# Kernel tuning notes

Measured on AMD Instinct MI355X. Metric: run time of the kernel, lower is better.

## Reference

```python
import jax, jax.numpy as jnp
import numpy as np

N = 50000   # num_nodes
E = 1600000 # edges (avg degree 32)
D = 256     # in_feats
H = 256     # n_hidden


def setup_inputs() -> dict:
    key = jax.random.key(0)
    ks = jax.random.split(key, 9)
    s = 1.0 / np.sqrt(D)
    return {
        "input_nodes": jnp.arange(N, dtype=jnp.int32),
        "edge_src": jax.random.randint(ks[0], (E,), 0, N, dtype=jnp.int32),
        "edge_dst": jax.random.randint(ks[1], (E,), 0, N, dtype=jnp.int32),
        "emb": jax.random.normal(ks[2], (N, D), jnp.float32) * 0.02,
        "W_self0": jax.random.normal(ks[3], (D, H), jnp.float32) * s,
        "W_neigh0": jax.random.normal(ks[4], (D, H), jnp.float32) * s,
        "b0": jnp.zeros((H,), jnp.float32),
        "W_self1": jax.random.normal(ks[5], (H, H), jnp.float32) * s,
        "W_neigh1": jax.random.normal(ks[6], (H, H), jnp.float32) * s,
        "b1": jnp.zeros((H,), jnp.float32),
    }


def _sage_mean(h, src, dst, W_self, W_neigh, b, n):
    # gather neighbor features, mean-reduce by destination, then linear.
    msgs = h[src]                                                  # [E, d]
    ssum = jax.ops.segment_sum(msgs, dst, num_segments=n)          # [n, d]
    deg = jax.ops.segment_sum(jnp.ones(src.shape, h.dtype), dst, num_segments=n)
    h_neigh = ssum / jnp.maximum(deg, 1.0)[:, None]
    return h @ W_self + h_neigh @ W_neigh + b


def reference(input_nodes, edge_src, edge_dst, emb,
              W_self0, W_neigh0, b0, W_self1, W_neigh1, b1):
    h = emb[input_nodes]                                            # [N, D]
    h = _sage_mean(h, edge_src, edge_dst, W_self0, W_neigh0, b0, N)
    h = jax.nn.relu(h)  # dropout is identity at inference
    h = _sage_mean(h, edge_src, edge_dst, W_self1, W_neigh1, b1, N)
    h = h / jnp.linalg.norm(h)  # global Frobenius norm, as in torch.norm(h)
    return h
```

## Files before the change

kernel.cpp:

```cpp
#include <hip/hip_runtime.h>
#include <math.h>

#define NN 50000
#define NE 1600000
#define DF 256
#define NBUCK 391

typedef unsigned short ushortT;
typedef __attribute__((ext_vector_type(8))) short short8;
typedef __attribute__((ext_vector_type(4))) float floatx4;

__device__ __forceinline__ unsigned bf16rne(float f) {
    unsigned u = __float_as_uint(f);
    return (u + 0x7fffu + ((u >> 16) & 1u)) >> 16;
}

#define ASYNC16(gptr, ldsptr) \
    __builtin_amdgcn_global_load_lds((const __attribute__((address_space(1))) unsigned*)(gptr), \
                                     (__attribute__((address_space(3))) unsigned*)(ldsptr), 16, 0, 0)


__global__ void k_zero(int* __restrict__ bcnt) {
    int i = blockIdx.x * 256 + threadIdx.x;
    if (i < NBUCK) bcnt[i] = 0;
}

__global__ __launch_bounds__(256)
void k_bhist(const int* __restrict__ dst, int* __restrict__ bcnt) {
    __shared__ int h[NBUCK];
    for (int i = threadIdx.x; i < NBUCK; i += 256) h[i] = 0;
    __syncthreads();
    int base = blockIdx.x * 4096;
#pragma unroll
    for (int i = 0; i < 16; ++i) {
        int e = base + i * 256 + threadIdx.x;
        if (e < NE) atomicAdd(&h[dst[e] >> 7], 1);
    }
    __syncthreads();
    for (int i = threadIdx.x; i < NBUCK; i += 256)
        if (h[i]) atomicAdd(&bcnt[i], h[i]);
}

__global__ void k_bscan(const int* __restrict__ bcnt, int* __restrict__ bbase,
                        int* __restrict__ cursor, int* __restrict__ row_ptr,
                        float* __restrict__ nrm) {
    __shared__ int s[512];
    int t = threadIdx.x;
    int v = (t < NBUCK) ? bcnt[t] : 0;
    s[t] = v; __syncthreads();
    for (int off = 1; off < 512; off <<= 1) {
        int x = (t >= off) ? s[t - off] : 0;
        __syncthreads();
        s[t] += x;
        __syncthreads();
    }
    if (t < NBUCK) { bbase[t] = s[t] - v; cursor[t] = s[t] - v; }
    if (t == 0) { bbase[NBUCK] = NE; row_ptr[NN] = NE; *nrm = 0.0f; }
}

__global__ __launch_bounds__(256)
void k_bin(const int* __restrict__ src, const int* __restrict__ dst,
           int* __restrict__ cursor, unsigned* __restrict__ rec) {
    __shared__ int h[NBUCK];
    __shared__ int gb[NBUCK];
    for (int i = threadIdx.x; i < NBUCK; i += 256) h[i] = 0;
    __syncthreads();
    const int base = blockIdx.x * 2048;
    int bk[8], rk[8];
    unsigned pk[8];
#pragma unroll
    for (int i = 0; i < 8; ++i) {
        int e = base + i * 256 + threadIdx.x;
        if (e < NE) {
            int d = dst[e];
            bk[i] = d >> 7;
            pk[i] = (unsigned)src[e] | ((unsigned)(d & 127) << 16);
            rk[i] = atomicAdd(&h[bk[i]], 1);
        } else bk[i] = -1;
    }
    __syncthreads();
    for (int i = threadIdx.x; i < NBUCK; i += 256) {
        int c = h[i];
        gb[i] = c ? atomicAdd(&cursor[i], c) : 0;
    }
    __syncthreads();
#pragma unroll
    for (int i = 0; i < 8; ++i)
        if (bk[i] >= 0) rec[gb[bk[i]] + rk[i]] = pk[i];
}

__global__ __launch_bounds__(256)
void k_csr(const unsigned* __restrict__ rec, const int* __restrict__ bbase,
           int* __restrict__ row_ptr, ushortT* __restrict__ csr) {
    __shared__ int cnt[128];
    __shared__ int cur[128];
    __shared__ int s[256];
    const int B = blockIdx.x, t = threadIdx.x;
    if (t < 128) cnt[t] = 0;
    __syncthreads();
    const int beg = bbase[B], end = bbase[B + 1];
    for (int p = beg + t; p < end; p += 256)
        atomicAdd(&cnt[(rec[p] >> 16) & 127], 1);
    __syncthreads();
    int v = (t < 128) ? cnt[t] : 0;
    s[t] = v; __syncthreads();
    for (int off = 1; off < 256; off <<= 1) {
        int x = (t >= off) ? s[t - off] : 0;
        __syncthreads();
        s[t] += x;
        __syncthreads();
    }
    if (t < 128) {
        int ex = s[t] - v;
        cur[t] = ex;
        int node = B * 128 + t;
        if (node < NN) row_ptr[node] = beg + ex;
    }
    __syncthreads();
    for (int p = beg + t; p < end; p += 256) {
        unsigned r = rec[p];
        int loc = atomicAdd(&cur[(r >> 16) & 127], 1);
        csr[beg + loc] = (ushortT)r;
    }
}


__global__ __launch_bounds__(256)
void k_cvt_emb(const float* __restrict__ emb, const int* __restrict__ gather,
               ushortT* __restrict__ out) {
    long long i = ((long long)blockIdx.x * 256 + threadIdx.x) * 8;
    int row = (int)(i >> 8);
    int col = (int)(i & 255);
    long long g = (long long)gather[row] * 256 + col;
    float4 v0 = *(const float4*)(emb + g);
    float4 v1 = *(const float4*)(emb + g + 4);
    uint4 o;
    o.x = bf16rne(v0.x) | (bf16rne(v0.y) << 16);
    o.y = bf16rne(v0.z) | (bf16rne(v0.w) << 16);
    o.z = bf16rne(v1.x) | (bf16rne(v1.y) << 16);
    o.w = bf16rne(v1.z) | (bf16rne(v1.w) << 16);
    *(uint4*)(out + i) = o;
}

__global__ __launch_bounds__(256)
void k_cvt_w(const float* __restrict__ Ws, const float* __restrict__ Wn,
             ushortT* __restrict__ Wt) {
    int idx = blockIdx.x * 256 + threadIdx.x;
    int n = idx >> 9;
    int k = idx & 511;
    float v = (k < 256) ? Ws[k * 256 + n] : Wn[(k - 256) * 256 + n];
    Wt[idx] = (ushortT)bf16rne(v);
}


__global__ __launch_bounds__(256)
void k_agg(const ushortT* __restrict__ feat, const int* __restrict__ row_ptr,
           const ushortT* __restrict__ csr, ushortT* __restrict__ out) {
    int node = blockIdx.x * 4 + (threadIdx.x >> 6);
    int lane = threadIdx.x & 63;
    int half = lane >> 5;
    int l5 = lane & 31;
    if (node >= NN) return;
    int beg = row_ptr[node], end = row_ptr[node + 1];

    float s[8] = {0.f, 0.f, 0.f, 0.f, 0.f, 0.f, 0.f, 0.f};
    int p = beg + half;

#define ACCUM(q) do { \
        s[0] += __uint_as_float(q.x << 16); \
        s[1] += __uint_as_float(q.x & 0xffff0000u); \
        s[2] += __uint_as_float(q.y << 16); \
        s[3] += __uint_as_float(q.y & 0xffff0000u); \
        s[4] += __uint_as_float(q.z << 16); \
        s[5] += __uint_as_float(q.z & 0xffff0000u); \
        s[6] += __uint_as_float(q.w << 16); \
        s[7] += __uint_as_float(q.w & 0xffff0000u); \
    } while (0)

    for (; p + 6 < end; p += 8) {
        long long r0 = (long long)csr[p]     * 256 + l5 * 8;
        long long r1 = (long long)csr[p + 2] * 256 + l5 * 8;
        long long r2 = (long long)csr[p + 4] * 256 + l5 * 8;
        long long r3 = (long long)csr[p + 6] * 256 + l5 * 8;
        uint4 a = *(const uint4*)(feat + r0);
        uint4 b = *(const uint4*)(feat + r1);
        uint4 c = *(const uint4*)(feat + r2);
        uint4 d = *(const uint4*)(feat + r3);
        ACCUM(a); ACCUM(b); ACCUM(c); ACCUM(d);
    }
    for (; p < end; p += 2) {
        long long r0 = (long long)csr[p] * 256 + l5 * 8;
        uint4 a = *(const uint4*)(feat + r0);
        ACCUM(a);
    }
#undef ACCUM

#pragma unroll
    for (int k = 0; k < 8; ++k) s[k] += __shfl_down(s[k], 32);

    if (half == 0) {
        float inv = 1.0f / fmaxf((float)(end - beg), 1.0f);
        uint4 o;
        o.x = bf16rne(s[0] * inv) | (bf16rne(s[1] * inv) << 16);
        o.y = bf16rne(s[2] * inv) | (bf16rne(s[3] * inv) << 16);
        o.z = bf16rne(s[4] * inv) | (bf16rne(s[5] * inv) << 16);
        o.w = bf16rne(s[6] * inv) | (bf16rne(s[7] * inv) << 16);
        *(uint4*)(out + (long long)node * 256 + l5 * 8) = o;
    }
}


template<int RELU, int NORM>
__global__ __launch_bounds__(256, 2)
void k_gemm(const ushortT* __restrict__ Aself, const ushortT* __restrict__ Aneigh,
            const ushortT* __restrict__ Wt, const float* __restrict__ bias,
            ushortT* __restrict__ Cb, float* __restrict__ Cf, float* __restrict__ norm_acc) {
    __shared__ ushortT As[4096];
    __shared__ ushortT Bs[4096];
    __shared__ float red[4];

    const int t = threadIdx.x;
    const int w = t >> 6;
    const int lane = t & 63;
    const int m0 = blockIdx.x * 128;
    const int n0 = blockIdx.y * 128;

    const int r0 = t >> 2;
    const int cu = (t & 3) * 8;

    const long long gA0 = (long long)min(m0 + r0, NN - 1) * 256;
    const long long gA1 = (long long)min(m0 + r0 + 64, NN - 1) * 256;
    const long long gB0 = (long long)(n0 + r0) * 512;
    const long long gB1 = (long long)(n0 + r0 + 64) * 512;

    const unsigned lds0 = w * 512;
    const unsigned lds1 = 2048 + w * 512;

    const int wm = w & 1, wn = w >> 1;
    const int fm = lane & 15;
    const int fk = (lane >> 4) * 8;

    floatx4 acc[4][4];
#pragma unroll
    for (int i = 0; i < 4; ++i)
#pragma unroll
        for (int j = 0; j < 4; ++j) acc[i][j] = (floatx4){0.f, 0.f, 0.f, 0.f};

    for (int kt = 0; kt < 512; kt += 32) {
        const ushortT* Ab; int kc;
        if (kt < 256) { Ab = Aself; kc = kt; } else { Ab = Aneigh; kc = kt - 256; }

        __syncthreads();
        ASYNC16(Ab + gA0 + kc + cu, As + lds0);
        ASYNC16(Ab + gA1 + kc + cu, As + lds1);
        ASYNC16(Wt + gB0 + kt + cu, Bs + lds0);
        ASYNC16(Wt + gB1 + kt + cu, Bs + lds1);
        __syncthreads();

        short8 af[4], bf[4];
#pragma unroll
        for (int i = 0; i < 4; ++i)
            af[i] = *(const short8*)&As[(wm * 64 + i * 16 + fm) * 32 + fk];
#pragma unroll
        for (int j = 0; j < 4; ++j)
            bf[j] = *(const short8*)&Bs[(wn * 64 + j * 16 + fm) * 32 + fk];
#pragma unroll
        for (int i = 0; i < 4; ++i)
#pragma unroll
            for (int j = 0; j < 4; ++j)
                acc[i][j] = __builtin_amdgcn_mfma_f32_16x16x32_bf16(af[i], bf[j], acc[i][j], 0, 0, 0);
    }

    float bj[4];
#pragma unroll
    for (int j = 0; j < 4; ++j) bj[j] = bias[n0 + wn * 64 + j * 16 + fm];

    float sumsq = 0.0f;
#pragma unroll
    for (int i = 0; i < 4; ++i) {
#pragma unroll
        for (int r = 0; r < 4; ++r) {
            const int row = m0 + wm * 64 + i * 16 + (lane >> 4) * 4 + r;
            if (row < NN) {
#pragma unroll
                for (int j = 0; j < 4; ++j) {
                    const int col = n0 + wn * 64 + j * 16 + fm;
                    float v = acc[i][j][r] + bj[j];
                    if (RELU) v = fmaxf(v, 0.0f);
                    if (NORM) {
                        Cf[(long long)row * 256 + col] = v;
                        sumsq += v * v;
                    } else {
                        Cb[(long long)row * 256 + col] = (ushortT)bf16rne(v);
                    }
                }
            }
        }
    }

    if (NORM) {
#pragma unroll
        for (int off = 32; off > 0; off >>= 1) sumsq += __shfl_down(sumsq, off);
        if (lane == 0) red[w] = sumsq;
        __syncthreads();
        if (t == 0) atomicAdd(norm_acc, red[0] + red[1] + red[2] + red[3]);
    }
}

__global__ void k_scale(float* __restrict__ out, const float* __restrict__ nrm) {
    const float s = 1.0f / sqrtf(*nrm);
    long long i = ((long long)blockIdx.x * 256 + threadIdx.x) * 4;
    float4 v = *(float4*)&out[i];
    v.x *= s; v.y *= s; v.z *= s; v.w *= s;
    *(float4*)&out[i] = v;
}


extern "C" void kernel_launch(void* const* d_in, const int* in_sizes, int n_in,
                              void* d_out, int out_size, void* d_ws, size_t ws_size,
                              hipStream_t stream) {
    const int*   input_nodes = (const int*)d_in[0];
    const int*   esrc = (const int*)d_in[1];
    const int*   edst = (const int*)d_in[2];
    const float* emb  = (const float*)d_in[3];
    const float* Ws0  = (const float*)d_in[4];
    const float* Wn0  = (const float*)d_in[5];
    const float* b0   = (const float*)d_in[6];
    const float* Ws1  = (const float*)d_in[7];
    const float* Wn1  = (const float*)d_in[8];
    const float* b1   = (const float*)d_in[9];
    float* out = (float*)d_out;

    char* base = (char*)d_ws;
    ushortT*  embb    = (ushortT*) (base);
    ushortT*  h1b     = (ushortT*) (base + 25600000);
    ushortT*  hnb     = (ushortT*) (base + 51200000);
    unsigned* rec     = (unsigned*)(base + 76800000);
    ushortT*  csr     = (ushortT*) (base + 83200000);
    ushortT*  Wt0     = (ushortT*) (base + 86400000);
    ushortT*  Wt1     = (ushortT*) (base + 86662144);
    int*      row_ptr = (int*)     (base + 86924288);
    int*      bcnt    = (int*)     (base + 87124304);
    int*      bbase   = (int*)     (base + 87125904);
    int*      cursor  = (int*)     (base + 87127504);
    float*    nrm     = (float*)   (base + 87129104);

    k_zero  <<<2,   256, 0, stream>>>(bcnt);
    k_bhist <<<391, 256, 0, stream>>>(edst, bcnt);
    k_bscan <<<1,   512, 0, stream>>>(bcnt, bbase, cursor, row_ptr, nrm);
    k_bin   <<<782, 256, 0, stream>>>(esrc, edst, cursor, rec);
    k_csr   <<<NBUCK, 256, 0, stream>>>(rec, bbase, row_ptr, csr);

    k_cvt_emb<<<NN * DF / 8 / 256, 256, 0, stream>>>(emb, input_nodes, embb);
    k_cvt_w  <<<512, 256, 0, stream>>>(Ws0, Wn0, Wt0);
    k_cvt_w  <<<512, 256, 0, stream>>>(Ws1, Wn1, Wt1);

    dim3 gg((NN + 127) / 128, 2);

    k_agg<<<NN / 4, 256, 0, stream>>>(embb, row_ptr, csr, hnb);
    k_gemm<1, 0><<<gg, 256, 0, stream>>>(embb, hnb, Wt0, b0, h1b, nullptr, nullptr);

    k_agg<<<NN / 4, 256, 0, stream>>>(h1b, row_ptr, csr, hnb);
    k_gemm<0, 1><<<gg, 256, 0, stream>>>(h1b, hnb, Wt1, b1, nullptr, out, nrm);

    k_scale<<<NN * DF / 4 / 256, 256, 0, stream>>>(out, nrm);
}
```

Before: 471.6 us.

## Fuse neighbor mean aggregation into GEMM via LDS-resident aggregated tile

```diff
diff --git a/kernel.cpp b/kernel.cpp
--- a/kernel.cpp
+++ b/kernel.cpp
@@ -153,19 +153,29 @@
 }
 
 
-__global__ __launch_bounds__(256)
-void k_agg(const ushortT* __restrict__ feat, const int* __restrict__ row_ptr,
-           const ushortT* __restrict__ csr, ushortT* __restrict__ out) {
-    int node = blockIdx.x * 4 + (threadIdx.x >> 6);
-    int lane = threadIdx.x & 63;
-    int half = lane >> 5;
-    int l5 = lane & 31;
-    if (node >= NN) return;
-    int beg = row_ptr[node], end = row_ptr[node + 1];
-
-    float s[8] = {0.f, 0.f, 0.f, 0.f, 0.f, 0.f, 0.f, 0.f};
-    int p = beg + half;
-
+template<int RELU, int NORM>
+__global__ __launch_bounds__(256, 2)
+void k_fused(const ushortT* __restrict__ A, const ushortT* __restrict__ Wt,
+             const float* __restrict__ bias, const int* __restrict__ row_ptr,
+             const ushortT* __restrict__ csr,
+             ushortT* __restrict__ Cb, float* __restrict__ Cf,
+             float* __restrict__ norm_acc) {
+    __shared__ ushortT S[40960];
+
+    const int t = threadIdx.x;
+    const int w = t >> 6;
+    const int lane = t & 63;
+    const int half = lane >> 5;
+    const int l5 = lane & 31;
+    const int m0 = blockIdx.x * 128;
+
+    for (int i = 0; i < 32; ++i) {
+        const int nl = w * 32 + i;
+        const int node = m0 + nl;
+        if (node >= NN) break;
+        const int beg = row_ptr[node], end = row_ptr[node + 1];
+        float s[8] = {0.f, 0.f, 0.f, 0.f, 0.f, 0.f, 0.f, 0.f};
+        int p = beg + half;
 #define ACCUM(q) do { \
         s[0] += __uint_as_float(q.x << 16); \
         s[1] += __uint_as_float(q.x & 0xffff0000u); \
@@ -176,122 +186,117 @@
         s[6] += __uint_as_float(q.w << 16); \
         s[7] += __uint_as_float(q.w & 0xffff0000u); \
     } while (0)
-
-    for (; p + 6 < end; p += 8) {
-        long long r0 = (long long)csr[p]     * 256 + l5 * 8;
-        long long r1 = (long long)csr[p + 2] * 256 + l5 * 8;
-        long long r2 = (long long)csr[p + 4] * 256 + l5 * 8;
-        long long r3 = (long long)csr[p + 6] * 256 + l5 * 8;
-        uint4 a = *(const uint4*)(feat + r0);
-        uint4 b = *(const uint4*)(feat + r1);
-        uint4 c = *(const uint4*)(feat + r2);
-        uint4 d = *(const uint4*)(feat + r3);
-        ACCUM(a); ACCUM(b); ACCUM(c); ACCUM(d);
-    }
-    for (; p < end; p += 2) {
-        long long r0 = (long long)csr[p] * 256 + l5 * 8;
-        uint4 a = *(const uint4*)(feat + r0);
-        ACCUM(a);
-    }
+        for (; p + 6 < end; p += 8) {
+            long long r0 = (long long)csr[p]     * 256 + l5 * 8;
+            long long r1 = (long long)csr[p + 2] * 256 + l5 * 8;
+            long long r2 = (long long)csr[p + 4] * 256 + l5 * 8;
+            long long r3 = (long long)csr[p + 6] * 256 + l5 * 8;
+            uint4 a = *(const uint4*)(A + r0);
+            uint4 b = *(const uint4*)(A + r1);
+            uint4 c = *(const uint4*)(A + r2);
+            uint4 d = *(const uint4*)(A + r3);
+            ACCUM(a); ACCUM(b); ACCUM(c); ACCUM(d);
+        }
+        for (; p < end; p += 2) {
+            long long r0 = (long long)csr[p] * 256 + l5 * 8;
+            uint4 a = *(const uint4*)(A + r0);
+            ACCUM(a);
+        }
 #undef ACCUM
-
-#pragma unroll
-    for (int k = 0; k < 8; ++k) s[k] += __shfl_down(s[k], 32);
-
-    if (half == 0) {
-        float inv = 1.0f / fmaxf((float)(end - beg), 1.0f);
-        uint4 o;
-        o.x = bf16rne(s[0] * inv) | (bf16rne(s[1] * inv) << 16);
-        o.y = bf16rne(s[2] * inv) | (bf16rne(s[3] * inv) << 16);
-        o.z = bf16rne(s[4] * inv) | (bf16rne(s[5] * inv) << 16);
-        o.w = bf16rne(s[6] * inv) | (bf16rne(s[7] * inv) << 16);
-        *(uint4*)(out + (long long)node * 256 + l5 * 8) = o;
-    }
-}
-
-
-template<int RELU, int NORM>
-__global__ __launch_bounds__(256, 2)
-void k_gemm(const ushortT* __restrict__ Aself, const ushortT* __restrict__ Aneigh,
-            const ushortT* __restrict__ Wt, const float* __restrict__ bias,
-            ushortT* __restrict__ Cb, float* __restrict__ Cf, float* __restrict__ norm_acc) {
-    __shared__ ushortT As[4096];
-    __shared__ ushortT Bs[4096];
-    __shared__ float red[4];
-
-    const int t = threadIdx.x;
-    const int w = t >> 6;
-    const int lane = t & 63;
-    const int m0 = blockIdx.x * 128;
-    const int n0 = blockIdx.y * 128;
+#pragma unroll
+        for (int k = 0; k < 8; ++k) s[k] += __shfl_down(s[k], 32);
+        if (half == 0) {
+            const float inv = 1.0f / fmaxf((float)(end - beg), 1.0f);
+            uint4 o;
+            o.x = bf16rne(s[0] * inv) | (bf16rne(s[1] * inv) << 16);
+            o.y = bf16rne(s[2] * inv) | (bf16rne(s[3] * inv) << 16);
+            o.z = bf16rne(s[4] * inv) | (bf16rne(s[5] * inv) << 16);
+            o.w = bf16rne(s[6] * inv) | (bf16rne(s[7] * inv) << 16);
+            *(uint4*)&S[(l5 >> 2) * 4096 + nl * 32 + (l5 & 3) * 8] = o;
+        }
+    }
+    __syncthreads();
 
     const int r0 = t >> 2;
     const int cu = (t & 3) * 8;
-
     const long long gA0 = (long long)min(m0 + r0, NN - 1) * 256;
     const long long gA1 = (long long)min(m0 + r0 + 64, NN - 1) * 256;
-    const long long gB0 = (long long)(n0 + r0) * 512;
-    const long long gB1 = (long long)(n0 + r0 + 64) * 512;
-
-    const unsigned lds0 = w * 512;
-    const unsigned lds1 = 2048 + w * 512;
+
+    const unsigned lA0 = 32768 + w * 512;
+    const unsigned lA1 = 32768 + 2048 + w * 512;
+    const unsigned lB0 = 36864 + w * 512;
+    const unsigned lB1 = 36864 + 2048 + w * 512;
 
     const int wm = w & 1, wn = w >> 1;
     const int fm = lane & 15;
     const int fk = (lane >> 4) * 8;
 
-    floatx4 acc[4][4];
-#pragma unroll
-    for (int i = 0; i < 4; ++i)
-#pragma unroll
-        for (int j = 0; j < 4; ++j) acc[i][j] = (floatx4){0.f, 0.f, 0.f, 0.f};
-
-    for (int kt = 0; kt < 512; kt += 32) {
-        const ushortT* Ab; int kc;
-        if (kt < 256) { Ab = Aself; kc = kt; } else { Ab = Aneigh; kc = kt - 256; }
-
-        __syncthreads();
-        ASYNC16(Ab + gA0 + kc + cu, As + lds0);
-        ASYNC16(Ab + gA1 + kc + cu, As + lds1);
-        ASYNC16(Wt + gB0 + kt + cu, Bs + lds0);
-        ASYNC16(Wt + gB1 + kt + cu, Bs + lds1);
-        __syncthreads();
-
-        short8 af[4], bf[4];
+    float sumsq = 0.0f;
+
+    for (int np = 0; np < 2; ++np) {
+        const int n0 = np * 128;
+        const int gB0 = (n0 + r0) * 512;
+        const int gB1 = (n0 + r0 + 64) * 512;
+
+        floatx4 acc[4][4];
 #pragma unroll
         for (int i = 0; i < 4; ++i)
-            af[i] = *(const short8*)&As[(wm * 64 + i * 16 + fm) * 32 + fk];
-#pragma unroll
-        for (int j = 0; j < 4; ++j)
-            bf[j] = *(const short8*)&Bs[(wn * 64 + j * 16 + fm) * 32 + fk];
-#pragma unroll
-        for (int i = 0; i < 4; ++i)
+#pragma unroll
+            for (int j = 0; j < 4; ++j) acc[i][j] = (floatx4){0.f, 0.f, 0.f, 0.f};
+
+        for (int kt = 0; kt < 512; kt += 32) {
+            const bool self = kt < 256;
+            __syncthreads();
+            if (self) {
+                ASYNC16(A + gA0 + kt + cu, S + lA0);
+                ASYNC16(A + gA1 + kt + cu, S + lA1);
+            }
+            ASYNC16(Wt + gB0 + kt + cu, S + lB0);
+            ASYNC16(Wt + gB1 + kt + cu, S + lB1);
+            __syncthreads();
+
+            short8 af[4], bf[4];
+            if (self) {
+#pragma unroll
+                for (int i = 0; i < 4; ++i)
+                    af[i] = *(const short8*)&S[32768 + (wm * 64 + i * 16 + fm) * 32 + fk];
+            } else {
+                const int kb = (kt - 256) >> 5;
+#pragma unroll
+                for (int i = 0; i < 4; ++i)
+                    af[i] = *(const short8*)&S[kb * 4096 + (wm * 64 + i * 16 + fm) * 32 + fk];
+            }
 #pragma unroll
             for (int j = 0; j < 4; ++j)
-                acc[i][j] = __builtin_amdgcn_mfma_f32_16x16x32_bf16(af[i], bf[j], acc[i][j], 0, 0, 0);
-    }
-
-    float bj[4];
-#pragma unroll
-    for (int j = 0; j < 4; ++j) bj[j] = bias[n0 + wn * 64 + j * 16 + fm];
-
-    float sumsq = 0.0f;
-#pragma unroll
-    for (int i = 0; i < 4; ++i) {
-#pragma unroll
-        for (int r = 0; r < 4; ++r) {
-            const int row = m0 + wm * 64 + i * 16 + (lane >> 4) * 4 + r;
-            if (row < NN) {
-#pragma unroll
-                for (int j = 0; j < 4; ++j) {
-                    const int col = n0 + wn * 64 + j * 16 + fm;
-                    float v = acc[i][j][r] + bj[j];
-                    if (RELU) v = fmaxf(v, 0.0f);
-                    if (NORM) {
-                        Cf[(long long)row * 256 + col] = v;
-                        sumsq += v * v;
-                    } else {
-                        Cb[(long long)row * 256 + col] = (ushortT)bf16rne(v);
+                bf[j] = *(const short8*)&S[36864 + (wn * 64 + j * 16 + fm) * 32 + fk];
+#pragma unroll
+            for (int i = 0; i < 4; ++i)
+#pragma unroll
+                for (int j = 0; j < 4; ++j)
+                    acc[i][j] = __builtin_amdgcn_mfma_f32_16x16x32_bf16(af[i], bf[j], acc[i][j], 0, 0, 0);
+        }
+
+        float bj[4];
+#pragma unroll
+        for (int j = 0; j < 4; ++j) bj[j] = bias[n0 + wn * 64 + j * 16 + fm];
+
+#pragma unroll
+        for (int i = 0; i < 4; ++i) {
+#pragma unroll
+            for (int r = 0; r < 4; ++r) {
+                const int row = m0 + wm * 64 + i * 16 + (lane >> 4) * 4 + r;
+                if (row < NN) {
+#pragma unroll
+                    for (int j = 0; j < 4; ++j) {
+                        const int col = n0 + wn * 64 + j * 16 + fm;
+                        float v = acc[i][j][r] + bj[j];
+                        if (RELU) v = fmaxf(v, 0.0f);
+                        if (NORM) {
+                            Cf[(long long)row * 256 + col] = v;
+                            sumsq += v * v;
+                        } else {
+                            Cb[(long long)row * 256 + col] = (ushortT)bf16rne(v);
+                        }
                     }
                 }
             }
@@ -301,6 +306,8 @@
     if (NORM) {
 #pragma unroll
         for (int off = 32; off > 0; off >>= 1) sumsq += __shfl_down(sumsq, off);
+        __syncthreads();
+        float* red = (float*)&S[32768];
         if (lane == 0) red[w] = sumsq;
         __syncthreads();
         if (t == 0) atomicAdd(norm_acc, red[0] + red[1] + red[2] + red[3]);
@@ -334,34 +341,28 @@
     char* base = (char*)d_ws;
     ushortT*  embb    = (ushortT*) (base);
     ushortT*  h1b     = (ushortT*) (base + 25600000);
-    ushortT*  hnb     = (ushortT*) (base + 51200000);
-    unsigned* rec     = (unsigned*)(base + 76800000);
-    ushortT*  csr     = (ushortT*) (base + 83200000);
-    ushortT*  Wt0     = (ushortT*) (base + 86400000);
-    ushortT*  Wt1     = (ushortT*) (base + 86662144);
-    int*      row_ptr = (int*)     (base + 86924288);
-    int*      bcnt    = (int*)     (base + 87124304);
-    int*      bbase   = (int*)     (base + 87125904);
-    int*      cursor  = (int*)     (base + 87127504);
-    float*    nrm     = (float*)   (base + 87129104);
-
-    k_zero  <<<2,   256, 0, stream>>>(bcnt);
-    k_bhist <<<391, 256, 0, stream>>>(edst, bcnt);
-    k_bscan <<<1,   512, 0, stream>>>(bcnt, bbase, cursor, row_ptr, nrm);
-    k_bin   <<<782, 256, 0, stream>>>(esrc, edst, cursor, rec);
+    unsigned* rec     = (unsigned*)(base + 51200000);
+    ushortT*  csr     = (ushortT*) (base + 57600000);
+    ushortT*  Wt0     = (ushortT*) (base + 60800000);
+    ushortT*  Wt1     = (ushortT*) (base + 61062144);
+    int*      row_ptr = (int*)     (base + 61324288);
+    int*      bcnt    = (int*)     (base + 61524304);
+    int*      bbase   = (int*)     (base + 61525904);
+    int*      cursor  = (int*)     (base + 61527504);
+    float*    nrm     = (float*)   (base + 61529104);
+
+    k_zero  <<<2,     256, 0, stream>>>(bcnt);
+    k_bhist <<<391,   256, 0, stream>>>(edst, bcnt);
+    k_bscan <<<1,     512, 0, stream>>>(bcnt, bbase, cursor, row_ptr, nrm);
+    k_bin   <<<782,   256, 0, stream>>>(esrc, edst, cursor, rec);
     k_csr   <<<NBUCK, 256, 0, stream>>>(rec, bbase, row_ptr, csr);
 
     k_cvt_emb<<<NN * DF / 8 / 256, 256, 0, stream>>>(emb, input_nodes, embb);
     k_cvt_w  <<<512, 256, 0, stream>>>(Ws0, Wn0, Wt0);
     k_cvt_w  <<<512, 256, 0, stream>>>(Ws1, Wn1, Wt1);
 
-    dim3 gg((NN + 127) / 128, 2);
-
-    k_agg<<<NN / 4, 256, 0, stream>>>(embb, row_ptr, csr, hnb);
-    k_gemm<1, 0><<<gg, 256, 0, stream>>>(embb, hnb, Wt0, b0, h1b, nullptr, nullptr);
-
-    k_agg<<<NN / 4, 256, 0, stream>>>(h1b, row_ptr, csr, hnb);
-    k_gemm<0, 1><<<gg, 256, 0, stream>>>(h1b, hnb, Wt1, b1, nullptr, out, nrm);
+    k_fused<1, 0><<<NBUCK, 256, 0, stream>>>(embb, Wt0, b0, row_ptr, csr, h1b, nullptr, nullptr);
+    k_fused<0, 1><<<NBUCK, 256, 0, stream>>>(h1b, Wt1, b1, row_ptr, csr, nullptr, out, nrm);
 
     k_scale<<<NN * DF / 4 / 256, 256, 0, stream>>>(out, nrm);
 }
```

Result: slower. 568.1 us (+20.5%).

## Retile GEMM to 64x256 blocks, merge conversion kernels, use 32-bit gather offsets

Applied to the files above, without the earlier changes.

```diff
diff --git a/kernel.cpp b/kernel.cpp
--- a/kernel.cpp
+++ b/kernel.cpp
@@ -126,30 +126,36 @@
 
 
 __global__ __launch_bounds__(256)
-void k_cvt_emb(const float* __restrict__ emb, const int* __restrict__ gather,
-               ushortT* __restrict__ out) {
-    long long i = ((long long)blockIdx.x * 256 + threadIdx.x) * 8;
-    int row = (int)(i >> 8);
-    int col = (int)(i & 255);
-    long long g = (long long)gather[row] * 256 + col;
-    float4 v0 = *(const float4*)(emb + g);
-    float4 v1 = *(const float4*)(emb + g + 4);
-    uint4 o;
-    o.x = bf16rne(v0.x) | (bf16rne(v0.y) << 16);
-    o.y = bf16rne(v0.z) | (bf16rne(v0.w) << 16);
-    o.z = bf16rne(v1.x) | (bf16rne(v1.y) << 16);
-    o.w = bf16rne(v1.z) | (bf16rne(v1.w) << 16);
-    *(uint4*)(out + i) = o;
-}
-
-__global__ __launch_bounds__(256)
-void k_cvt_w(const float* __restrict__ Ws, const float* __restrict__ Wn,
-             ushortT* __restrict__ Wt) {
-    int idx = blockIdx.x * 256 + threadIdx.x;
-    int n = idx >> 9;
-    int k = idx & 511;
-    float v = (k < 256) ? Ws[k * 256 + n] : Wn[(k - 256) * 256 + n];
-    Wt[idx] = (ushortT)bf16rne(v);
+void k_cvt(const float* __restrict__ emb, const int* __restrict__ gather,
+           ushortT* __restrict__ embb,
+           const float* __restrict__ Ws0, const float* __restrict__ Wn0,
+           ushortT* __restrict__ Wt0,
+           const float* __restrict__ Ws1, const float* __restrict__ Wn1,
+           ushortT* __restrict__ Wt1) {
+    const int b = blockIdx.x;
+    if (b < 6250) {
+        long long i = ((long long)b * 256 + threadIdx.x) * 8;
+        int row = (int)(i >> 8);
+        int col = (int)(i & 255);
+        long long g = (long long)gather[row] * 256 + col;
+        float4 v0 = *(const float4*)(emb + g);
+        float4 v1 = *(const float4*)(emb + g + 4);
+        uint4 o;
+        o.x = bf16rne(v0.x) | (bf16rne(v0.y) << 16);
+        o.y = bf16rne(v0.z) | (bf16rne(v0.w) << 16);
+        o.z = bf16rne(v1.x) | (bf16rne(v1.y) << 16);
+        o.w = bf16rne(v1.z) | (bf16rne(v1.w) << 16);
+        *(uint4*)(embb + i) = o;
+    } else {
+        const bool first = b < 6762;
+        const int idx = ((first ? b - 6250 : b - 6762)) * 256 + threadIdx.x;
+        const int n = idx >> 9;
+        const int k = idx & 511;
+        const float* Ws = first ? Ws0 : Ws1;
+        const float* Wn = first ? Wn0 : Wn1;
+        float v = (k < 256) ? Ws[k * 256 + n] : Wn[(k - 256) * 256 + n];
+        (first ? Wt0 : Wt1)[idx] = (ushortT)bf16rne(v);
+    }
 }
 
 
@@ -178,10 +184,10 @@
     } while (0)
 
     for (; p + 6 < end; p += 8) {
-        long long r0 = (long long)csr[p]     * 256 + l5 * 8;
-        long long r1 = (long long)csr[p + 2] * 256 + l5 * 8;
-        long long r2 = (long long)csr[p + 4] * 256 + l5 * 8;
-        long long r3 = (long long)csr[p + 6] * 256 + l5 * 8;
+        int r0 = (int)csr[p]     * DF + l5 * 8;
+        int r1 = (int)csr[p + 2] * DF + l5 * 8;
+        int r2 = (int)csr[p + 4] * DF + l5 * 8;
+        int r3 = (int)csr[p + 6] * DF + l5 * 8;
         uint4 a = *(const uint4*)(feat + r0);
         uint4 b = *(const uint4*)(feat + r1);
         uint4 c = *(const uint4*)(feat + r2);
@@ -189,7 +195,7 @@
         ACCUM(a); ACCUM(b); ACCUM(c); ACCUM(d);
     }
     for (; p < end; p += 2) {
-        long long r0 = (long long)csr[p] * 256 + l5 * 8;
+        int r0 = (int)csr[p] * DF + l5 * 8;
         uint4 a = *(const uint4*)(feat + r0);
         ACCUM(a);
     }
@@ -205,38 +211,33 @@
         o.y = bf16rne(s[2] * inv) | (bf16rne(s[3] * inv) << 16);
         o.z = bf16rne(s[4] * inv) | (bf16rne(s[5] * inv) << 16);
         o.w = bf16rne(s[6] * inv) | (bf16rne(s[7] * inv) << 16);
-        *(uint4*)(out + (long long)node * 256 + l5 * 8) = o;
+        *(uint4*)(out + (long long)node * DF + l5 * 8) = o;
     }
 }
 
 
 template<int RELU, int NORM>
-__global__ __launch_bounds__(256, 2)
+__global__ __launch_bounds__(256, 4)
 void k_gemm(const ushortT* __restrict__ Aself, const ushortT* __restrict__ Aneigh,
             const ushortT* __restrict__ Wt, const float* __restrict__ bias,
             ushortT* __restrict__ Cb, float* __restrict__ Cf, float* __restrict__ norm_acc) {
-    __shared__ ushortT As[4096];
-    __shared__ ushortT Bs[4096];
+    __shared__ ushortT As[2048];
+    __shared__ ushortT Bs[8192];
     __shared__ float red[4];
 
     const int t = threadIdx.x;
     const int w = t >> 6;
     const int lane = t & 63;
-    const int m0 = blockIdx.x * 128;
-    const int n0 = blockIdx.y * 128;
-
-    const int r0 = t >> 2;
+    const int m0 = blockIdx.x * 64;
+
+    const int ar = t >> 2;
     const int cu = (t & 3) * 8;
 
-    const long long gA0 = (long long)min(m0 + r0, NN - 1) * 256;
-    const long long gA1 = (long long)min(m0 + r0 + 64, NN - 1) * 256;
-    const long long gB0 = (long long)(n0 + r0) * 512;
-    const long long gB1 = (long long)(n0 + r0 + 64) * 512;
-
-    const unsigned lds0 = w * 512;
-    const unsigned lds1 = 2048 + w * 512;
-
-    const int wm = w & 1, wn = w >> 1;
+    const long long gA = (long long)min(m0 + ar, NN - 1) * 256;
+
+    const unsigned ldsA = w * 512;
+    const unsigned ldsB = w * 512;
+
     const int fm = lane & 15;
     const int fk = (lane >> 4) * 8;
 
@@ -251,19 +252,19 @@
         if (kt < 256) { Ab = Aself; kc = kt; } else { Ab = Aneigh; kc = kt - 256; }
 
         __syncthreads();
-        ASYNC16(Ab + gA0 + kc + cu, As + lds0);
-        ASYNC16(Ab + gA1 + kc + cu, As + lds1);
-        ASYNC16(Wt + gB0 + kt + cu, Bs + lds0);
-        ASYNC16(Wt + gB1 + kt + cu, Bs + lds1);
+        ASYNC16(Ab + gA + kc + cu, As + ldsA);
+#pragma unroll
+        for (int i = 0; i < 4; ++i)
+            ASYNC16(Wt + (i * 64 + ar) * 512 + kt + cu, Bs + i * 2048 + ldsB);
         __syncthreads();
 
         short8 af[4], bf[4];
 #pragma unroll
         for (int i = 0; i < 4; ++i)
-            af[i] = *(const short8*)&As[(wm * 64 + i * 16 + fm) * 32 + fk];
+            af[i] = *(const short8*)&As[(i * 16 + fm) * 32 + fk];
 #pragma unroll
         for (int j = 0; j < 4; ++j)
-            bf[j] = *(const short8*)&Bs[(wn * 64 + j * 16 + fm) * 32 + fk];
+            bf[j] = *(const short8*)&Bs[(w * 64 + j * 16 + fm) * 32 + fk];
 #pragma unroll
         for (int i = 0; i < 4; ++i)
 #pragma unroll
@@ -273,18 +274,18 @@
 
     float bj[4];
 #pragma unroll
-    for (int j = 0; j < 4; ++j) bj[j] = bias[n0 + wn * 64 + j * 16 + fm];
+    for (int j = 0; j < 4; ++j) bj[j] = bias[w * 64 + j * 16 + fm];
 
     float sumsq = 0.0f;
 #pragma unroll
     for (int i = 0; i < 4; ++i) {
 #pragma unroll
         for (int r = 0; r < 4; ++r) {
-            const int row = m0 + wm * 64 + i * 16 + (lane >> 4) * 4 + r;
+            const int row = m0 + i * 16 + (lane >> 4) * 4 + r;
             if (row < NN) {
 #pragma unroll
                 for (int j = 0; j < 4; ++j) {
-                    const int col = n0 + wn * 64 + j * 16 + fm;
+                    const int col = w * 64 + j * 16 + fm;
                     float v = acc[i][j][r] + bj[j];
                     if (RELU) v = fmaxf(v, 0.0f);
                     if (NORM) {
@@ -345,23 +346,21 @@
     int*      cursor  = (int*)     (base + 87127504);
     float*    nrm     = (float*)   (base + 87129104);
 
-    k_zero  <<<2,   256, 0, stream>>>(bcnt);
-    k_bhist <<<391, 256, 0, stream>>>(edst, bcnt);
-    k_bscan <<<1,   512, 0, stream>>>(bcnt, bbase, cursor, row_ptr, nrm);
-    k_bin   <<<782, 256, 0, stream>>>(esrc, edst, cursor, rec);
+    k_zero  <<<2,     256, 0, stream>>>(bcnt);
+    k_bhist <<<391,   256, 0, stream>>>(edst, bcnt);
+    k_bscan <<<1,     512, 0, stream>>>(bcnt, bbase, cursor, row_ptr, nrm);
+    k_bin   <<<782,   256, 0, stream>>>(esrc, edst, cursor, rec);
     k_csr   <<<NBUCK, 256, 0, stream>>>(rec, bbase, row_ptr, csr);
 
-    k_cvt_emb<<<NN * DF / 8 / 256, 256, 0, stream>>>(emb, input_nodes, embb);
-    k_cvt_w  <<<512, 256, 0, stream>>>(Ws0, Wn0, Wt0);
-    k_cvt_w  <<<512, 256, 0, stream>>>(Ws1, Wn1, Wt1);
-
-    dim3 gg((NN + 127) / 128, 2);
+    k_cvt<<<7274, 256, 0, stream>>>(emb, input_nodes, embb, Ws0, Wn0, Wt0, Ws1, Wn1, Wt1);
+
+    const int GEMM_BLOCKS = (NN + 63) / 64;
 
     k_agg<<<NN / 4, 256, 0, stream>>>(embb, row_ptr, csr, hnb);
-    k_gemm<1, 0><<<gg, 256, 0, stream>>>(embb, hnb, Wt0, b0, h1b, nullptr, nullptr);
+    k_gemm<1, 0><<<GEMM_BLOCKS, 256, 0, stream>>>(embb, hnb, Wt0, b0, h1b, nullptr, nullptr);
 
     k_agg<<<NN / 4, 256, 0, stream>>>(h1b, row_ptr, csr, hnb);
-    k_gemm<0, 1><<<gg, 256, 0, stream>>>(h1b, hnb, Wt1, b1, nullptr, out, nrm);
+    k_gemm<0, 1><<<GEMM_BLOCKS, 256, 0, stream>>>(h1b, hnb, Wt1, b1, nullptr, out, nrm);
 
     k_scale<<<NN * DF / 4 / 256, 256, 0, stream>>>(out, nrm);
 }
```

Result: no change. 467.7 us (-0.8%).
